# Kernel optimization log

Measured on AMD Instinct MI355X. Metric: run time of the kernel, lower is better.

The kernel has to match this reference:

```python
import jax, jax.numpy as jnp
import numpy as np

NEG_SLOPE = 0.2  # PyG GATConv default negative_slope
EPS = 1e-16     # PyG softmax denominator epsilon
NUM_GRAPHS = 64


def gat_layer(h_in, src, dst, W, att_src, att_dst, bias):
    """One PyG-style GATConv (concat heads, self-loops already in src/dst).
    h_in: [N, F_in]; W: [F_in, H*C]; att_src/att_dst: [H, C]; bias: [H*C].
    Returns [N, H*C]."""
    N = h_in.shape[0]
    H, C = att_src.shape
    h = (h_in @ W).reshape(N, H, C)                      # [N,H,C]
    a_src = jnp.einsum('nhc,hc->nh', h, att_src)          # [N,H]
    a_dst = jnp.einsum('nhc,hc->nh', h, att_dst)          # [N,H]
    e = jax.nn.leaky_relu(a_src[src] + a_dst[dst], NEG_SLOPE)  # [E,H]
    # numerically-stable softmax over edges grouped by destination node
    m = jax.ops.segment_max(e, dst, num_segments=N)
    m = jnp.where(jnp.isfinite(m), m, 0.0)
    ex = jnp.exp(e - m[dst])
    denom = jax.ops.segment_sum(ex, dst, num_segments=N)
    alpha = ex / (denom[dst] + EPS)                       # [E,H]
    msg = h[src] * alpha[:, :, None]                      # [E,H,C]
    out = jax.ops.segment_sum(msg, dst, num_segments=N)   # [N,H,C]
    return out.reshape(N, H * C) + bias


def setup_inputs() -> dict:
    key = jax.random.key(0)
    ks = jax.random.split(key, 20)
    N, E, F_in, H, C, B, O = 50000, 800000, 128, 4, 64, NUM_GRAPHS, 16
    x = jax.random.normal(ks[0], (N, F_in), dtype=jnp.float32)
    edge_index = jax.random.randint(ks[1], (2, E), 0, N, dtype=jnp.int32)
    batch_index = jnp.sort(jax.random.randint(ks[2], (N,), 0, B, dtype=jnp.int32))

    def lin(k, fi, fo):
        return jax.random.normal(k, (fi, fo), jnp.float32) / np.float32(np.sqrt(fi))

    def att(k):
        return jax.random.normal(k, (H, C), jnp.float32) * np.float32(0.1)

    return {
        'x': x, 'edge_index': edge_index, 'batch_index': batch_index,
        'W0': lin(ks[3], F_in, H * C), 'a0s': att(ks[4]), 'a0d': att(ks[5]), 'b0': jnp.zeros((H * C,), jnp.float32),
        'W1': lin(ks[6], H * C, H * C), 'a1s': att(ks[7]), 'a1d': att(ks[8]), 'b1': jnp.zeros((H * C,), jnp.float32),
        'W2': lin(ks[9], H * C, H * C), 'a2s': att(ks[10]), 'a2d': att(ks[11]), 'b2': jnp.zeros((H * C,), jnp.float32),
        'Wout': lin(ks[12], 3 * C, O), 'bout': jnp.zeros((O,), jnp.float32),
    }


def reference(x, edge_index, batch_index, W0, a0s, a0d, b0, W1, a1s, a1d, b1,
              W2, a2s, a2d, b2, Wout, bout):
    N = x.shape[0]
    H, C = a0s.shape
    loops = jnp.arange(N, dtype=edge_index.dtype)         # PyG add_self_loops=True
    src = jnp.concatenate([edge_index[0], loops])
    dst = jnp.concatenate([edge_index[1], loops])

    h = x
    for (W, a_s, a_d, b) in ((W0, a0s, a0d, b0), (W1, a1s, a1d, b1), (W2, a2s, a2d, b2)):
        h = jnp.tanh(gat_layer(h, src, dst, W, a_s, a_d, b))

    node = h.reshape(N, H, C).mean(axis=1)                # mean over heads -> [N,C]
    B = NUM_GRAPHS
    gmax = jax.ops.segment_max(node, batch_index, num_segments=B)
    gsum = jax.ops.segment_sum(node, batch_index, num_segments=B)
    cnt = jax.ops.segment_sum(jnp.ones((N, 1), node.dtype), batch_index, num_segments=B)
    gmean = gsum / jnp.maximum(cnt, 1.0)
    hidden = jnp.concatenate([gmax, gmean, gsum], axis=1)  # [B, 3C]
    # dropout p=0.5 is identity in eval mode
    out = hidden @ Wout + bout
    return out, hidden
```

## Files before the change

### kernel.cpp

```cpp
#include <hip/hip_runtime.h>
#include <cfloat>
#include <cmath>

#define NEG_SLOPE 0.2f
#define SOFT_EPS 1e-16f
#define LOG2E 1.4426950408889634f

typedef __bf16 bf16_t;
typedef bf16_t bf16x8 __attribute__((ext_vector_type(8)));
typedef float floatx4 __attribute__((ext_vector_type(4)));
typedef float floatx2 __attribute__((ext_vector_type(2)));

__device__ __forceinline__ float leaky(float x) { return fmaxf(x, NEG_SLOPE * x); }

__device__ __forceinline__ float fast_exp(float x) {
  return __builtin_amdgcn_exp2f(x * LOG2E);
}
__device__ __forceinline__ float fast_tanh(float x) {
  float xc = fminf(fmaxf(x, -15.f), 15.f);
  float t = __builtin_amdgcn_exp2f(xc * (2.f * LOG2E));
  return 1.f - 2.f * __builtin_amdgcn_rcpf(t + 1.f);
}

__device__ __forceinline__ unsigned short f2bf(float f) {
  unsigned u = __float_as_uint(f);
  unsigned r = u + 0x7fffu + ((u >> 16) & 1u);
  return (unsigned short)(r >> 16);
}

__device__ __forceinline__ unsigned enc_f(float f) {
  unsigned u = __float_as_uint(f);
  return (u & 0x80000000u) ? ~u : (u | 0x80000000u);
}
__device__ __forceinline__ float dec_f(unsigned e) {
  unsigned u = (e & 0x80000000u) ? (e ^ 0x80000000u) : ~e;
  return __uint_as_float(u);
}

__global__ void count_deg(const int* __restrict__ ei, int E, int N, int* __restrict__ counts) {
  int e = blockIdx.x * blockDim.x + threadIdx.x;
  int Etot = E + N;
  if (e >= Etot) return;
  int d = (e < E) ? ei[E + e] : (e - E);
  atomicAdd(&counts[d], 1);
}

__global__ __launch_bounds__(256) void chunk_sum(const int* __restrict__ counts,
                                                 int* __restrict__ chunkSum, int N) {
  __shared__ int sc[256];
  int b = blockIdx.x, t = threadIdx.x;
  int base = b * 2048 + t * 8;
  int s = 0;
#pragma unroll
  for (int i = 0; i < 8; ++i) { int idx = base + i; if (idx < N) s += counts[idx]; }
  sc[t] = s; __syncthreads();
  for (int o = 128; o > 0; o >>= 1) { if (t < o) sc[t] += sc[t + o]; __syncthreads(); }
  if (t == 0) chunkSum[b] = sc[0];
}

__global__ void scan_chunks(const int* __restrict__ chunkSum, int* __restrict__ chunkOff,
                            int nb, int* __restrict__ row_start, int N, int Etot,
                            unsigned* __restrict__ gmax, float* __restrict__ gsum,
                            int* __restrict__ cnt) {
  int t = threadIdx.x;
  for (int i = t; i < 64 * 64; i += 64) { gmax[i] = 0x007FFFFFu; gsum[i] = 0.f; }
  cnt[t] = 0;
  if (t == 0) {
    int r = 0;
    for (int b = 0; b < nb; ++b) { chunkOff[b] = r; r += chunkSum[b]; }
    row_start[N] = Etot;
  }
}

__global__ __launch_bounds__(256) void scan_emit(const int* __restrict__ counts,
    const int* __restrict__ chunkOff, int* __restrict__ row_start,
    int* __restrict__ write_ptr, int N) {
  __shared__ int sc[256];
  int b = blockIdx.x, t = threadIdx.x;
  int base = b * 2048 + t * 8;
  int v[8]; int s = 0;
#pragma unroll
  for (int i = 0; i < 8; ++i) { int idx = base + i; v[i] = (idx < N) ? counts[idx] : 0; s += v[i]; }
  sc[t] = s; __syncthreads();
  for (int o = 1; o < 256; o <<= 1) {
    int x = (t >= o) ? sc[t - o] : 0;
    __syncthreads();
    sc[t] += x;
    __syncthreads();
  }
  int run = chunkOff[b] + sc[t] - s;
#pragma unroll
  for (int i = 0; i < 8; ++i) {
    int idx = base + i;
    if (idx < N) { row_start[idx] = run; write_ptr[idx] = run; }
    run += v[i];
  }
}

__global__ void scatter_edges(const int* __restrict__ ei, int E, int N,
                              int* __restrict__ write_ptr, int2* __restrict__ edge_sd) {
  int e = blockIdx.x * blockDim.x + threadIdx.x;
  int Etot = E + N;
  if (e >= Etot) return;
  int s, d;
  if (e < E) { s = ei[e]; d = ei[E + e]; } else { s = e - E; d = e - E; }
  int pos = atomicAdd(&write_ptr[d], 1);
  edge_sd[pos] = make_int2(s, d);
}

__global__ __launch_bounds__(256) void cvt_bf16(const float* __restrict__ in,
                                                unsigned short* __restrict__ out, int n4) {
  int i = blockIdx.x * 256 + threadIdx.x;
  if (i >= n4) return;
  float4 v = ((const float4*)in)[i];
  ushort4 o;
  o.x = f2bf(v.x); o.y = f2bf(v.y); o.z = f2bf(v.z); o.w = f2bf(v.w);
  ((ushort4*)out)[i] = o;
}

__global__ __launch_bounds__(256) void cvt_wt3(const float* __restrict__ W0,
    const float* __restrict__ W1, const float* __restrict__ W2,
    unsigned short* __restrict__ T0, unsigned short* __restrict__ T1,
    unsigned short* __restrict__ T2, int K0) {
  const float* W; unsigned short* T; int K;
  if (blockIdx.z == 0)      { W = W0; T = T0; K = K0; }
  else if (blockIdx.z == 1) { W = W1; T = T1; K = 256; }
  else                      { W = W2; T = T2; K = 256; }
  int tx = threadIdx.x & 15, ty = threadIdx.x >> 4;
  int k = blockIdx.x * 16 + tx;
  int n = blockIdx.y * 16 + ty;
  if (k < K) T[(size_t)n * K + k] = f2bf(W[(size_t)k * 256 + n]);
}

#define BM 128
#define BN 128
#define BK 64

__global__ __launch_bounds__(256) void gemm_core(const unsigned short* __restrict__ A,
    const unsigned short* __restrict__ Bt, unsigned char* __restrict__ Cout8,
    float* __restrict__ a_src, float* __restrict__ a_dst,
    const float* __restrict__ attS, const float* __restrict__ attD, int N, int K) {
  __shared__ __align__(16) unsigned char ldsraw[34304];
  unsigned short* ldsbuf = (unsigned short*)ldsraw;
  int t = threadIdx.x;
  int wave = t >> 6, lane = t & 63;
  int wm = wave & 1, wn = wave >> 1;
  int row0 = blockIdx.y * BM;
  int col0 = blockIdx.x * BN;
  floatx4 acc[4][4] = {};

  int rbase = (lane & 15);
  int kq8 = (lane >> 4) * 8;

  for (int k0 = 0; k0 < K; k0 += BK) {
#pragma unroll
    for (int rr = 0; rr < 4; ++rr) {
      int R = wave * 4 + rr;
      int grow = row0 + (R >> 1) * 16 + rbase;
      int gk = k0 + (R & 1) * 32 + kq8;
      const unsigned short* ga = A + (size_t)grow * K + gk;
      __builtin_amdgcn_global_load_lds(
          (const __attribute__((address_space(1))) void*)ga,
          (__attribute__((address_space(3))) void*)(ldsbuf + R * 512), 16, 0, 0);
      int gcol = col0 + (R >> 1) * 16 + rbase;
      const unsigned short* gb = Bt + (size_t)gcol * K + gk;
      __builtin_amdgcn_global_load_lds(
          (const __attribute__((address_space(1))) void*)gb,
          (__attribute__((address_space(3))) void*)(ldsbuf + 8192 + R * 512), 16, 0, 0);
    }
    __syncthreads();
#pragma unroll
    for (int ks = 0; ks < 2; ++ks) {
      bf16x8 af[4], bfr[4];
#pragma unroll
      for (int i = 0; i < 4; ++i)
        af[i] = *(const bf16x8*)(ldsbuf + ((wm * 4 + i) * 2 + ks) * 512 + lane * 8);
#pragma unroll
      for (int j = 0; j < 4; ++j)
        bfr[j] = *(const bf16x8*)(ldsbuf + 8192 + ((wn * 4 + j) * 2 + ks) * 512 + lane * 8);
#pragma unroll
      for (int i = 0; i < 4; ++i)
#pragma unroll
        for (int j = 0; j < 4; ++j)
          acc[i][j] = __builtin_amdgcn_mfma_f32_16x16x32_bf16(af[i], bfr[j], acc[i][j], 0, 0, 0);
    }
    __syncthreads();
  }

  int head = blockIdx.x * 2 + wn;
  int cin = lane & 15;
  float aS[4], aD[4];
#pragma unroll
  for (int j = 0; j < 4; ++j) {
    aS[j] = attS[head * 64 + j * 16 + cin];
    aD[j] = attD[head * 64 + j * 16 + cin];
  }
#pragma unroll
  for (int i = 0; i < 4; ++i) {
    floatx4 ps = {0.f, 0.f, 0.f, 0.f}, pd = {0.f, 0.f, 0.f, 0.f};
#pragma unroll
    for (int j = 0; j < 4; ++j) {
      ps += acc[i][j] * aS[j];
      pd += acc[i][j] * aD[j];
    }
#pragma unroll
    for (int m = 1; m < 16; m <<= 1) {
#pragma unroll
      for (int k = 0; k < 4; ++k) {
        ps[k] += __shfl_xor(ps[k], m, 64);
        pd[k] += __shfl_xor(pd[k], m, 64);
      }
    }
    if ((lane & 15) == 0) {
      int rb = row0 + wm * 64 + i * 16 + (lane >> 4) * 4;
#pragma unroll
      for (int reg = 0; reg < 4; ++reg) {
        int r = rb + reg;
        if (r < N) {
          a_src[r * 4 + head] = ps[reg];
          a_dst[r * 4 + head] = pd[reg];
        }
      }
    }
  }

  float* ldsf = (float*)ldsraw;
#pragma unroll
  for (int p = 0; p < 2; ++p) {
    __syncthreads();
    if (wm == p) {
#pragma unroll
      for (int i = 0; i < 4; ++i) {
        int rloc = i * 16 + (lane >> 4) * 4;
#pragma unroll
        for (int j = 0; j < 4; ++j) {
          int col = wn * 64 + j * 16 + (lane & 15);
#pragma unroll
          for (int reg = 0; reg < 4; ++reg)
            ldsf[(rloc + reg) * 132 + col] = acc[i][j][reg];
        }
      }
    }
    __syncthreads();
    int browbase = row0 + p * 64;
#pragma unroll
    for (int q = 0; q < 2; ++q) {
      int idx = t + 256 * q;
      int prow = idx >> 3;
      int cb = (idx & 7) * 16;
      int grow = browbase + prow;
      if (grow < N) {
        const float* fp = &ldsf[prow * 132 + cb];
        unsigned ov[4];
#pragma unroll
        for (int q4 = 0; q4 < 4; ++q4) {
          unsigned v = 0;
          v = __builtin_amdgcn_cvt_pk_fp8_f32(fp[q4 * 4 + 0], fp[q4 * 4 + 1], v, false);
          v = __builtin_amdgcn_cvt_pk_fp8_f32(fp[q4 * 4 + 2], fp[q4 * 4 + 3], v, true);
          ov[q4] = v;
        }
        *(uint4*)(Cout8 + (size_t)grow * 256 + col0 + cb) =
            make_uint4(ov[0], ov[1], ov[2], ov[3]);
      }
    }
  }
}

__global__ __launch_bounds__(256) void attn_agg(const unsigned char* __restrict__ g8,
    const float* __restrict__ a_src, const float* __restrict__ a_dst,
    const int* __restrict__ row_start, const int2* __restrict__ edge_sd,
    const float* __restrict__ bias,
    unsigned short* __restrict__ hout_bf, float* __restrict__ nodemean, int N) {
  __shared__ float els[4][64 * 4];
  int lane = threadIdx.x & 63;
  int w = threadIdx.x >> 6;
  int n = blockIdx.x * 4 + w;
  if (n >= N) return;
  int beg = row_start[n], end = row_start[n + 1];
  float* ew = els[w];

  float4 adn = *(const float4*)(a_dst + (size_t)n * 4);

  float4 dv = make_float4(0.f, 0.f, 0.f, 0.f);
  for (int i = beg + lane; i < end; i += 64) {
    int s = edge_sd[i].x;
    float4 as = *(const float4*)(a_src + (size_t)s * 4);
    float4 ev;
    ev.x = fast_exp(fminf(leaky(as.x + adn.x), 60.f));
    ev.y = fast_exp(fminf(leaky(as.y + adn.y), 60.f));
    ev.z = fast_exp(fminf(leaky(as.z + adn.z), 60.f));
    ev.w = fast_exp(fminf(leaky(as.w + adn.w), 60.f));
    int idx = i - beg;
    if (idx < 64) *(float4*)(&ew[idx * 4]) = ev;
    dv.x += ev.x; dv.y += ev.y; dv.z += ev.z; dv.w += ev.w;
  }
  for (int m = 1; m < 64; m <<= 1) {
    dv.x += __shfl_xor(dv.x, m, 64);
    dv.y += __shfl_xor(dv.y, m, 64);
    dv.z += __shfl_xor(dv.z, m, 64);
    dv.w += __shfl_xor(dv.w, m, 64);
  }

  int half = lane >> 5;
  int l = lane & 31;
  int h = l >> 3;
  int c0 = l * 8;
  float den = (h == 0) ? dv.x : (h == 1) ? dv.y : (h == 2) ? dv.z : dv.w;
  float adh = (h == 0) ? adn.x : (h == 1) ? adn.y : (h == 2) ? adn.z : adn.w;
  float invh = __builtin_amdgcn_rcpf(den + SOFT_EPS);

  auto EG = [&](int i) -> float {
    int idx = i - beg;
    if (idx < 64) return ew[idx * 4 + h];
    int s = edge_sd[i].x;
    return fast_exp(fminf(leaky(a_src[(size_t)s * 4 + h] + adh), 60.f));
  };

  floatx2 p0 = {0.f, 0.f}, p1 = {0.f, 0.f}, p2 = {0.f, 0.f}, p3 = {0.f, 0.f};
  int i = beg + half;
  for (; i + 6 < end; i += 8) {
    int s0 = edge_sd[i].x;
    int s1 = edge_sd[i + 2].x;
    int s2 = edge_sd[i + 4].x;
    int s3 = edge_sd[i + 6].x;
    float e0 = EG(i);
    float e1 = EG(i + 2);
    float e2 = EG(i + 4);
    float e3 = EG(i + 6);
    uint2 g0 = *(const uint2*)(g8 + (size_t)s0 * 256 + c0);
    uint2 g1 = *(const uint2*)(g8 + (size_t)s1 * 256 + c0);
    uint2 g2 = *(const uint2*)(g8 + (size_t)s2 * 256 + c0);
    uint2 g3 = *(const uint2*)(g8 + (size_t)s3 * 256 + c0);
    p0 += e0 * (floatx2)__builtin_amdgcn_cvt_pk_f32_fp8(g0.x, false)
        + e1 * (floatx2)__builtin_amdgcn_cvt_pk_f32_fp8(g1.x, false)
        + e2 * (floatx2)__builtin_amdgcn_cvt_pk_f32_fp8(g2.x, false)
        + e3 * (floatx2)__builtin_amdgcn_cvt_pk_f32_fp8(g3.x, false);
    p1 += e0 * (floatx2)__builtin_amdgcn_cvt_pk_f32_fp8(g0.x, true)
        + e1 * (floatx2)__builtin_amdgcn_cvt_pk_f32_fp8(g1.x, true)
        + e2 * (floatx2)__builtin_amdgcn_cvt_pk_f32_fp8(g2.x, true)
        + e3 * (floatx2)__builtin_amdgcn_cvt_pk_f32_fp8(g3.x, true);
    p2 += e0 * (floatx2)__builtin_amdgcn_cvt_pk_f32_fp8(g0.y, false)
        + e1 * (floatx2)__builtin_amdgcn_cvt_pk_f32_fp8(g1.y, false)
        + e2 * (floatx2)__builtin_amdgcn_cvt_pk_f32_fp8(g2.y, false)
        + e3 * (floatx2)__builtin_amdgcn_cvt_pk_f32_fp8(g3.y, false);
    p3 += e0 * (floatx2)__builtin_amdgcn_cvt_pk_f32_fp8(g0.y, true)
        + e1 * (floatx2)__builtin_amdgcn_cvt_pk_f32_fp8(g1.y, true)
        + e2 * (floatx2)__builtin_amdgcn_cvt_pk_f32_fp8(g2.y, true)
        + e3 * (floatx2)__builtin_amdgcn_cvt_pk_f32_fp8(g3.y, true);
  }
  for (; i < end; i += 2) {
    int s = edge_sd[i].x;
    float e0 = EG(i);
    uint2 gv = *(const uint2*)(g8 + (size_t)s * 256 + c0);
    p0 += e0 * (floatx2)__builtin_amdgcn_cvt_pk_f32_fp8(gv.x, false);
    p1 += e0 * (floatx2)__builtin_amdgcn_cvt_pk_f32_fp8(gv.x, true);
    p2 += e0 * (floatx2)__builtin_amdgcn_cvt_pk_f32_fp8(gv.y, false);
    p3 += e0 * (floatx2)__builtin_amdgcn_cvt_pk_f32_fp8(gv.y, true);
  }
  float a0 = p0[0], a1 = p0[1], a2 = p1[0], a3 = p1[1];
  float a4 = p2[0], a5 = p2[1], a6 = p3[0], a7 = p3[1];
  a0 += __shfl_xor(a0, 32, 64); a1 += __shfl_xor(a1, 32, 64);
  a2 += __shfl_xor(a2, 32, 64); a3 += __shfl_xor(a3, 32, 64);
  a4 += __shfl_xor(a4, 32, 64); a5 += __shfl_xor(a5, 32, 64);
  a6 += __shfl_xor(a6, 32, 64); a7 += __shfl_xor(a7, 32, 64);
  a0 *= invh; a1 *= invh; a2 *= invh; a3 *= invh;
  a4 *= invh; a5 *= invh; a6 *= invh; a7 *= invh;

  float4 b01 = *(const float4*)(bias + c0);
  float4 b23 = *(const float4*)(bias + c0 + 4);
  float o0 = fast_tanh(a0 + b01.x), o1 = fast_tanh(a1 + b01.y);
  float o2 = fast_tanh(a2 + b01.z), o3 = fast_tanh(a3 + b01.w);
  float o4 = fast_tanh(a4 + b23.x), o5 = fast_tanh(a5 + b23.y);
  float o6 = fast_tanh(a6 + b23.z), o7 = fast_tanh(a7 + b23.w);

  if (hout_bf) {
    if (half == 0) {
      unsigned q0 = (unsigned)f2bf(o0) | ((unsigned)f2bf(o1) << 16);
      unsigned q1 = (unsigned)f2bf(o2) | ((unsigned)f2bf(o3) << 16);
      unsigned q2 = (unsigned)f2bf(o4) | ((unsigned)f2bf(o5) << 16);
      unsigned q3 = (unsigned)f2bf(o6) | ((unsigned)f2bf(o7) << 16);
      *(uint4*)(hout_bf + (size_t)n * 256 + c0) = make_uint4(q0, q1, q2, q3);
    }
  } else {
    o0 += __shfl_xor(o0, 8, 64);  o1 += __shfl_xor(o1, 8, 64);
    o2 += __shfl_xor(o2, 8, 64);  o3 += __shfl_xor(o3, 8, 64);
    o4 += __shfl_xor(o4, 8, 64);  o5 += __shfl_xor(o5, 8, 64);
    o6 += __shfl_xor(o6, 8, 64);  o7 += __shfl_xor(o7, 8, 64);
    o0 += __shfl_xor(o0, 16, 64); o1 += __shfl_xor(o1, 16, 64);
    o2 += __shfl_xor(o2, 16, 64); o3 += __shfl_xor(o3, 16, 64);
    o4 += __shfl_xor(o4, 16, 64); o5 += __shfl_xor(o5, 16, 64);
    o6 += __shfl_xor(o6, 16, 64); o7 += __shfl_xor(o7, 16, 64);
    if (half == 0 && l < 8) {
      float* np = nodemean + (size_t)n * 64 + l * 8;
      *(float4*)(np)     = make_float4(0.25f * o0, 0.25f * o1, 0.25f * o2, 0.25f * o3);
      *(float4*)(np + 4) = make_float4(0.25f * o4, 0.25f * o5, 0.25f * o6, 0.25f * o7);
    }
  }
}

#define RNPB 256
__global__ __launch_bounds__(256) void readout_nodes(const float* __restrict__ nm,
    const int* __restrict__ batch, unsigned* __restrict__ gmax,
    float* __restrict__ gsum, int* __restrict__ cnt, int N) {
  int t = threadIdx.x;
  int c = t & 63;
  int q = t >> 6;
  int n0 = blockIdx.x * RNPB + q * (RNPB / 4);
  if (n0 >= N) return;
  int n1 = min(n0 + RNPB / 4, N);
  float vmax = -FLT_MAX, vsum = 0.f;
  int curb = batch[n0];
  int cl = 0;
  for (int n = n0; n < n1; ++n) {
    int b = batch[n];
    if (b != curb) {
      atomicMax(&gmax[curb * 64 + c], enc_f(vmax));
      atomicAdd(&gsum[curb * 64 + c], vsum);
      if (c == 0) atomicAdd(&cnt[curb], cl);
      vmax = -FLT_MAX; vsum = 0.f; cl = 0; curb = b;
    }
    float v = nm[(size_t)n * 64 + c];
    vmax = fmaxf(vmax, v); vsum += v; ++cl;
  }
  atomicMax(&gmax[curb * 64 + c], enc_f(vmax));
  atomicAdd(&gsum[curb * 64 + c], vsum);
  if (c == 0) atomicAdd(&cnt[curb], cl);
}

__global__ __launch_bounds__(256) void finalize(const unsigned* __restrict__ gmax,
    const float* __restrict__ gsum, const int* __restrict__ cnt,
    const float* __restrict__ Wout, const float* __restrict__ bout,
    float* __restrict__ out) {
  __shared__ float hid[64 * 192];
  int t = threadIdx.x;
  for (int i = t; i < 64 * 192; i += 256) {
    int b = i / 192, j = i % 192;
    float v;
    if (j < 64) v = dec_f(gmax[b * 64 + j]);
    else if (j < 128) v = gsum[b * 64 + j - 64] / fmaxf((float)cnt[b], 1.f);
    else v = gsum[b * 64 + j - 128];
    hid[i] = v;
    out[1024 + i] = v;
  }
  __syncthreads();
  for (int i = t; i < 64 * 16; i += 256) {
    int b = i >> 4, o = i & 15;
    float s = bout[o];
    for (int k = 0; k < 192; ++k) s += hid[b * 192 + k] * Wout[k * 16 + o];
    out[i] = s;
  }
}

extern "C" void kernel_launch(void* const* d_in, const int* in_sizes, int n_in,
                              void* d_out, int out_size, void* d_ws, size_t ws_size,
                              hipStream_t stream) {
  const float* x     = (const float*)d_in[0];
  const int*   ei    = (const int*)d_in[1];
  const int*   batch = (const int*)d_in[2];
  const float* W[3]  = {(const float*)d_in[3], (const float*)d_in[7], (const float*)d_in[11]};
  const float* as_[3] = {(const float*)d_in[4], (const float*)d_in[8], (const float*)d_in[12]};
  const float* ad_[3] = {(const float*)d_in[5], (const float*)d_in[9], (const float*)d_in[13]};
  const float* bb[3] = {(const float*)d_in[6], (const float*)d_in[10], (const float*)d_in[14]};
  const float* Wout  = (const float*)d_in[15];
  const float* bout  = (const float*)d_in[16];
  float* out = (float*)d_out;

  int N    = in_sizes[2];
  int Fin  = in_sizes[0] / N;
  int E    = in_sizes[1] / 2;
  int Etot = E + N;

  char* ws = (char*)d_ws;
  size_t off = 0;
  auto alloc = [&](size_t bytes) -> void* {
    void* p = ws + off;
    off += bytes;
    off = (off + 255) & ~(size_t)255;
    return p;
  };
  unsigned char* gbuf  = (unsigned char*)alloc((size_t)N * 256);
  unsigned short* h0bf = (unsigned short*)alloc((size_t)N * Fin * 2);
  unsigned short* h1bf = (unsigned short*)alloc((size_t)N * 256 * 2);
  float* nodemean  = (float*)alloc((size_t)N * 64 * 4);
  unsigned short* Wt[3];
  Wt[0] = (unsigned short*)alloc((size_t)256 * Fin * 2);
  Wt[1] = (unsigned short*)alloc((size_t)256 * 256 * 2);
  Wt[2] = (unsigned short*)alloc((size_t)256 * 256 * 2);
  float* a_src    = (float*)alloc((size_t)N * 4 * 4);
  float* a_dst    = (float*)alloc((size_t)N * 4 * 4);
  int* counts     = (int*)alloc((size_t)N * 4);
  int* row_start  = (int*)alloc((size_t)(N + 1) * 4);
  int* write_ptr  = (int*)alloc((size_t)N * 4);
  int2* edge_sd   = (int2*)alloc((size_t)Etot * 8);
  int* chunkSum   = (int*)alloc(64 * 4);
  int* chunkOff   = (int*)alloc(64 * 4);
  unsigned* gmax  = (unsigned*)alloc(64 * 64 * 4);
  float* gsum     = (float*)alloc(64 * 64 * 4);
  int* cnt        = (int*)alloc(64 * 4);

  hipMemsetAsync(counts, 0, (size_t)N * 4, stream);
  int nb = (N + 2047) / 2048;
  count_deg<<<(Etot + 255) / 256, 256, 0, stream>>>(ei, E, N, counts);
  chunk_sum<<<nb, 256, 0, stream>>>(counts, chunkSum, N);
  scan_chunks<<<1, 64, 0, stream>>>(chunkSum, chunkOff, nb, row_start, N, Etot,
                                    gmax, gsum, cnt);
  scan_emit<<<nb, 256, 0, stream>>>(counts, chunkOff, row_start, write_ptr, N);
  scatter_edges<<<(Etot + 255) / 256, 256, 0, stream>>>(ei, E, N, write_ptr, edge_sd);

  cvt_wt3<<<dim3(16, 16, 3), 256, 0, stream>>>(W[0], W[1], W[2], Wt[0], Wt[1], Wt[2], Fin);
  cvt_bf16<<<((N * Fin / 4) + 255) / 256, 256, 0, stream>>>(x, h0bf, N * Fin / 4);

  const unsigned short* Ain = h0bf;
  int K = Fin;
  for (int l = 0; l < 3; ++l) {
    dim3 gg(2, (N + BM - 1) / BM);
    gemm_core<<<gg, 256, 0, stream>>>(Ain, Wt[l], gbuf, a_src, a_dst,
                                      as_[l], ad_[l], N, K);
    attn_agg<<<(N + 3) / 4, 256, 0, stream>>>(gbuf, a_src, a_dst, row_start, edge_sd,
                                              bb[l],
                                              (l < 2) ? h1bf : (unsigned short*)nullptr,
                                              (l == 2) ? nodemean : (float*)nullptr, N);
    Ain = h1bf;
    K = 256;
  }

  readout_nodes<<<(N + RNPB - 1) / RNPB, 256, 0, stream>>>(nodemean, batch, gmax, gsum, cnt, N);
  finalize<<<1, 256, 0, stream>>>(gmax, gsum, cnt, Wout, bout, out);
}
```

Measured before the change: 512.9 us.

## Keep weight tile resident in LDS and stream row strips per wave

```diff
diff --git a/kernel.cpp b/kernel.cpp
--- a/kernel.cpp
+++ b/kernel.cpp
@@ -132,135 +132,94 @@
   if (k < K) T[(size_t)n * K + k] = f2bf(W[(size_t)k * 256 + n]);
 }
 
-#define BM 128
-#define BN 128
-#define BK 64
-
-__global__ __launch_bounds__(256) void gemm_core(const unsigned short* __restrict__ A,
-    const unsigned short* __restrict__ Bt, unsigned char* __restrict__ Cout8,
+template<int KK>
+__global__ __launch_bounds__(256) void gemm_resident(const unsigned short* __restrict__ A,
+    const unsigned short* __restrict__ Bt, unsigned char* __restrict__ g8,
     float* __restrict__ a_src, float* __restrict__ a_dst,
-    const float* __restrict__ attS, const float* __restrict__ attD, int N, int K) {
-  __shared__ __align__(16) unsigned char ldsraw[34304];
-  unsigned short* ldsbuf = (unsigned short*)ldsraw;
+    const float* __restrict__ attS, const float* __restrict__ attD, int N) {
+  constexpr int KC = KK / 32;
+  __shared__ __align__(16) unsigned short ldsB[8 * KC * 512];
   int t = threadIdx.x;
   int wave = t >> 6, lane = t & 63;
-  int wm = wave & 1, wn = wave >> 1;
-  int row0 = blockIdx.y * BM;
-  int col0 = blockIdx.x * BN;
-  floatx4 acc[4][4] = {};
-
-  int rbase = (lane & 15);
-  int kq8 = (lane >> 4) * 8;
-
-  for (int k0 = 0; k0 < K; k0 += BK) {
-#pragma unroll
-    for (int rr = 0; rr < 4; ++rr) {
-      int R = wave * 4 + rr;
-      int grow = row0 + (R >> 1) * 16 + rbase;
-      int gk = k0 + (R & 1) * 32 + kq8;
-      const unsigned short* ga = A + (size_t)grow * K + gk;
-      __builtin_amdgcn_global_load_lds(
-          (const __attribute__((address_space(1))) void*)ga,
-          (__attribute__((address_space(3))) void*)(ldsbuf + R * 512), 16, 0, 0);
-      int gcol = col0 + (R >> 1) * 16 + rbase;
-      const unsigned short* gb = Bt + (size_t)gcol * K + gk;
-      __builtin_amdgcn_global_load_lds(
-          (const __attribute__((address_space(1))) void*)gb,
-          (__attribute__((address_space(3))) void*)(ldsbuf + 8192 + R * 512), 16, 0, 0);
-    }
-    __syncthreads();
-#pragma unroll
-    for (int ks = 0; ks < 2; ++ks) {
-      bf16x8 af[4], bfr[4];
-#pragma unroll
-      for (int i = 0; i < 4; ++i)
-        af[i] = *(const bf16x8*)(ldsbuf + ((wm * 4 + i) * 2 + ks) * 512 + lane * 8);
-#pragma unroll
-      for (int j = 0; j < 4; ++j)
-        bfr[j] = *(const bf16x8*)(ldsbuf + 8192 + ((wn * 4 + j) * 2 + ks) * 512 + lane * 8);
-#pragma unroll
-      for (int i = 0; i < 4; ++i)
-#pragma unroll
-        for (int j = 0; j < 4; ++j)
-          acc[i][j] = __builtin_amdgcn_mfma_f32_16x16x32_bf16(af[i], bfr[j], acc[i][j], 0, 0, 0);
-    }
-    __syncthreads();
-  }
-
-  int head = blockIdx.x * 2 + wn;
   int cin = lane & 15;
-  float aS[4], aD[4];
-#pragma unroll
-  for (int j = 0; j < 4; ++j) {
-    aS[j] = attS[head * 64 + j * 16 + cin];
-    aD[j] = attD[head * 64 + j * 16 + cin];
-  }
-#pragma unroll
-  for (int i = 0; i < 4; ++i) {
-    floatx4 ps = {0.f, 0.f, 0.f, 0.f}, pd = {0.f, 0.f, 0.f, 0.f};
-#pragma unroll
-    for (int j = 0; j < 4; ++j) {
-      ps += acc[i][j] * aS[j];
-      pd += acc[i][j] * aD[j];
-    }
-#pragma unroll
-    for (int m = 1; m < 16; m <<= 1) {
-#pragma unroll
-      for (int k = 0; k < 4; ++k) {
-        ps[k] += __shfl_xor(ps[k], m, 64);
-        pd[k] += __shfl_xor(pd[k], m, 64);
+  int qr = lane >> 4;
+  int gb = blockIdx.x * 128;
+
+  for (int r = wave; r < 8 * KC; r += 4) {
+    int j = r / KC, kc = r % KC;
+    const unsigned short* src = Bt + (size_t)(gb + j * 16 + cin) * KK + kc * 32 + qr * 8;
+    __builtin_amdgcn_global_load_lds(
+        (const __attribute__((address_space(1))) void*)src,
+        (__attribute__((address_space(3))) void*)(ldsB + r * 512), 16, 0, 0);
+  }
+  __syncthreads();
+
+  float aSv[2][4], aDv[2][4];
+#pragma unroll
+  for (int hh = 0; hh < 2; ++hh)
+#pragma unroll
+    for (int jj = 0; jj < 4; ++jj) {
+      aSv[hh][jj] = attS[(blockIdx.x * 2 + hh) * 64 + jj * 16 + cin];
+      aDv[hh][jj] = attD[(blockIdx.x * 2 + hh) * 64 + jj * 16 + cin];
+    }
+
+  int NS = (N + 15) >> 4;
+  for (int s = blockIdx.y * 4 + wave; s < NS; s += 1024) {
+    int row0 = s * 16;
+    const unsigned short* arow = A + (size_t)(row0 + cin) * KK + qr * 8;
+    bf16x8 av[KC];
+#pragma unroll
+    for (int kc = 0; kc < KC; ++kc)
+      av[kc] = *(const bf16x8*)(arow + kc * 32);
+    floatx4 acc[8] = {};
+#pragma unroll
+    for (int kc = 0; kc < KC; ++kc) {
+#pragma unroll
+      for (int j = 0; j < 8; ++j) {
+        bf16x8 bv = *(const bf16x8*)(ldsB + (j * KC + kc) * 512 + lane * 8);
+        acc[j] = __builtin_amdgcn_mfma_f32_16x16x32_bf16(av[kc], bv, acc[j], 0, 0, 0);
       }
     }
-    if ((lane & 15) == 0) {
-      int rb = row0 + wm * 64 + i * 16 + (lane >> 4) * 4;
-#pragma unroll
-      for (int reg = 0; reg < 4; ++reg) {
-        int r = rb + reg;
-        if (r < N) {
-          a_src[r * 4 + head] = ps[reg];
-          a_dst[r * 4 + head] = pd[reg];
+
+#pragma unroll
+    for (int hh = 0; hh < 2; ++hh) {
+      floatx4 ps = {0.f, 0.f, 0.f, 0.f}, pd = {0.f, 0.f, 0.f, 0.f};
+#pragma unroll
+      for (int jj = 0; jj < 4; ++jj) {
+        int j = hh * 4 + jj;
+        ps += acc[j] * aSv[hh][jj];
+        pd += acc[j] * aDv[hh][jj];
+      }
+#pragma unroll
+      for (int m = 1; m < 16; m <<= 1)
+#pragma unroll
+        for (int k = 0; k < 4; ++k) {
+          ps[k] += __shfl_xor(ps[k], m, 64);
+          pd[k] += __shfl_xor(pd[k], m, 64);
+        }
+      if (cin == 0) {
+        int head = blockIdx.x * 2 + hh;
+#pragma unroll
+        for (int reg = 0; reg < 4; ++reg) {
+          int row = row0 + qr * 4 + reg;
+          if (row < N) {
+            a_src[row * 4 + head] = ps[reg];
+            a_dst[row * 4 + head] = pd[reg];
+          }
         }
       }
     }
-  }
-
-  float* ldsf = (float*)ldsraw;
-#pragma unroll
-  for (int p = 0; p < 2; ++p) {
-    __syncthreads();
-    if (wm == p) {
-#pragma unroll
-      for (int i = 0; i < 4; ++i) {
-        int rloc = i * 16 + (lane >> 4) * 4;
-#pragma unroll
-        for (int j = 0; j < 4; ++j) {
-          int col = wn * 64 + j * 16 + (lane & 15);
-#pragma unroll
-          for (int reg = 0; reg < 4; ++reg)
-            ldsf[(rloc + reg) * 132 + col] = acc[i][j][reg];
+
+#pragma unroll
+    for (int j = 0; j < 8; ++j) {
+      int col = gb + j * 16 + cin;
+#pragma unroll
+      for (int reg = 0; reg < 4; ++reg) {
+        int row = row0 + qr * 4 + reg;
+        if (row < N) {
+          unsigned v = __builtin_amdgcn_cvt_pk_fp8_f32(acc[j][reg], acc[j][reg], 0u, false);
+          g8[(size_t)row * 256 + col] = (unsigned char)(v & 0xffu);
         }
-      }
-    }
-    __syncthreads();
-    int browbase = row0 + p * 64;
-#pragma unroll
-    for (int q = 0; q < 2; ++q) {
-      int idx = t + 256 * q;
-      int prow = idx >> 3;
-      int cb = (idx & 7) * 16;
-      int grow = browbase + prow;
-      if (grow < N) {
-        const float* fp = &ldsf[prow * 132 + cb];
-        unsigned ov[4];
-#pragma unroll
-        for (int q4 = 0; q4 < 4; ++q4) {
-          unsigned v = 0;
-          v = __builtin_amdgcn_cvt_pk_fp8_f32(fp[q4 * 4 + 0], fp[q4 * 4 + 1], v, false);
-          v = __builtin_amdgcn_cvt_pk_fp8_f32(fp[q4 * 4 + 2], fp[q4 * 4 + 3], v, true);
-          ov[q4] = v;
-        }
-        *(uint4*)(Cout8 + (size_t)grow * 256 + col0 + cb) =
-            make_uint4(ov[0], ov[1], ov[2], ov[3]);
       }
     }
   }
@@ -511,17 +470,19 @@
   cvt_bf16<<<((N * Fin / 4) + 255) / 256, 256, 0, stream>>>(x, h0bf, N * Fin / 4);
 
   const unsigned short* Ain = h0bf;
-  int K = Fin;
   for (int l = 0; l < 3; ++l) {
-    dim3 gg(2, (N + BM - 1) / BM);
-    gemm_core<<<gg, 256, 0, stream>>>(Ain, Wt[l], gbuf, a_src, a_dst,
-                                      as_[l], ad_[l], N, K);
+    dim3 gg(2, 256);
+    if (l == 0 && Fin == 128)
+      gemm_resident<128><<<gg, 256, 0, stream>>>(Ain, Wt[l], gbuf, a_src, a_dst,
+                                                 as_[l], ad_[l], N);
+    else
+      gemm_resident<256><<<gg, 256, 0, stream>>>(Ain, Wt[l], gbuf, a_src, a_dst,
+                                                 as_[l], ad_[l], N);
     attn_agg<<<(N + 3) / 4, 256, 0, stream>>>(gbuf, a_src, a_dst, row_start, edge_sd,
                                               bb[l],
                                               (l < 2) ? h1bf : (unsigned short*)nullptr,
                                               (l == 2) ? nodemean : (float*)nullptr, N);
     Ain = h1bf;
-    K = 256;
   }
 
   readout_nodes<<<(N + RNPB - 1) / RNPB, 256, 0, stream>>>(nodemean, batch, gmax, gsum, cnt, N);
```

Result: slower. 535.8 us (+4.5%).
